# Kernel optimization log

Measured on AMD Instinct MI355X. Metric: run time of the kernel, lower is better.

The kernel has to match this reference:

```python
import jax, jax.numpy as jnp
import numpy as np

N = 50000   # nodes
E = 800000  # edges
D = 64      # d_in = d_h = d_out
H1 = 8      # GAT layer-1 heads


def _self_loops(src, dst, n):
    loop = jnp.arange(n)
    return jnp.concatenate([src, loop]), jnp.concatenate([dst, loop])


def gcn_conv(x, src, dst, W, b):
    # PyG GCNConv: symmetric normalization with self-loops, bias added last.
    n = x.shape[0]
    h = x @ W
    s, d = _self_loops(src, dst, n)
    deg = jax.ops.segment_sum(jnp.ones(s.shape[0], h.dtype), d, num_segments=n)
    dinv = jnp.where(deg > 0, deg ** -0.5, 0.0)
    norm = dinv[s] * dinv[d]                                   # [E+N]
    out = jax.ops.segment_sum(h[s] * norm[:, None], d, num_segments=n)
    return out + b


def sage_conv(x, src, dst, Wl, bl, Wr):
    # PyG SAGEConv: mean neighbor aggregation -> lin_l, plus root -> lin_r.
    n = x.shape[0]
    msg = jax.ops.segment_sum(x[src], dst, num_segments=n)
    cnt = jax.ops.segment_sum(jnp.ones(src.shape[0], x.dtype), dst, num_segments=n)
    mean = msg / jnp.maximum(cnt, 1.0)[:, None]
    return mean @ Wl + bl + x @ Wr


def gat_conv(x, src, dst, W, a_src, a_dst, b, heads):
    # PyG GATConv: per-head additive attention, self-loops, segment softmax, concat.
    n = x.shape[0]
    h = (x @ W).reshape(n, heads, -1)                          # [N,H,C]
    al_s = (h * a_src).sum(-1)                                 # [N,H]
    al_d = (h * a_dst).sum(-1)                                 # [N,H]
    s, d = _self_loops(src, dst, n)
    e = jax.nn.leaky_relu(al_s[s] + al_d[d], 0.2)              # [E',H]
    emax = jax.ops.segment_max(e, d, num_segments=n)           # [N,H]
    ex = jnp.exp(e - emax[d])
    den = jax.ops.segment_sum(ex, d, num_segments=n)
    alpha = ex / (den[d] + 1e-16)                              # [E',H]
    out = jax.ops.segment_sum(h[s] * alpha[:, :, None], d, num_segments=n)
    return out.reshape(n, -1) + b


def relu_res(h):
    # get_hiddens: rh = h before ReLU module, then h = relu(h) + rh
    return jax.nn.relu(h) + h


def layer_norm(x, g, b, eps=1e-6):
    mu = x.mean(-1, keepdims=True)
    var = ((x - mu) ** 2).mean(-1, keepdims=True)
    return (x - mu) * jax.lax.rsqrt(var + eps) * g + b


def setup_inputs():
    key = jax.random.key(0)
    ks = jax.random.split(key, 16)
    sc = 1.0 / np.sqrt(D)
    return {
        "x": jax.random.normal(ks[0], (N, D), jnp.float32),
        "edge_index": jax.random.randint(ks[1], (2, E), 0, N),
        "batch": jnp.sort(jax.random.randint(ks[2], (N,), 0, 64)),
        "gcn_W": jax.random.normal(ks[3], (3, D, D), jnp.float32) * sc,
        "gcn_b": jnp.zeros((3, D), jnp.float32),
        "sage_Wl": jax.random.normal(ks[4], (3, D, D), jnp.float32) * sc,
        "sage_bl": jnp.zeros((3, D), jnp.float32),
        "sage_Wr": jax.random.normal(ks[5], (3, D, D), jnp.float32) * sc,
        "gat1_W": jax.random.normal(ks[6], (D, D), jnp.float32) * sc,
        "gat1_asrc": jax.random.normal(ks[7], (H1, D // H1), jnp.float32) * sc,
        "gat1_adst": jax.random.normal(ks[8], (H1, D // H1), jnp.float32) * sc,
        "gat1_b": jnp.zeros((D,), jnp.float32),
        "gat2_W": jax.random.normal(ks[9], (D, D), jnp.float32) * sc,
        "gat2_asrc": jax.random.normal(ks[10], (1, D), jnp.float32) * sc,
        "gat2_adst": jax.random.normal(ks[11], (1, D), jnp.float32) * sc,
        "gat2_b": jnp.zeros((D,), jnp.float32),
        "ln_g": jnp.ones((D,), jnp.float32),
        "ln_b": jnp.zeros((D,), jnp.float32),
    }


def reference(x, edge_index, batch, gcn_W, gcn_b, sage_Wl, sage_bl, sage_Wr,
              gat1_W, gat1_asrc, gat1_adst, gat1_b,
              gat2_W, gat2_asrc, gat2_adst, gat2_b, ln_g, ln_b):
    src, dst = edge_index[0], edge_index[1]
    # channel 0: sz_l=3 GCNConv stack
    h = x
    for l in range(3):
        h = relu_res(gcn_conv(h, src, dst, gcn_W[l], gcn_b[l]))
    c_gcn = h
    # channel 1: GAT(8 heads) -> GAT(1 head)
    h = relu_res(gat_conv(x, src, dst, gat1_W, gat1_asrc, gat1_adst, gat1_b, H1))
    h = relu_res(gat_conv(h, src, dst, gat2_W, gat2_asrc, gat2_adst, gat2_b, 1))
    c_gat = h
    # channel 2: sz_l=3 SAGEConv stack
    h = x
    for l in range(3):
        h = relu_res(sage_conv(h, src, dst, sage_Wl[l], sage_bl[l], sage_Wr[l]))
    c_sage = h
    channal = jnp.stack([c_gcn, c_gat, c_sage])                # [3,N,d_out]
    out = layer_norm(channal, ln_g, ln_b)
    batchs = jnp.ones((3, batch.shape[0]), jnp.float32) * batch.astype(jnp.float32)
    return out, batchs
```

## Files before the change

kernel.cpp:

```cpp
#include <hip/hip_runtime.h>
#include <hip/hip_bf16.h>

typedef __hip_bfloat16 bf16;

static inline int ceil_div(long long a, int b) { return (int)((a + b - 1) / b); }

__device__ __forceinline__ float ld(const void* p, long long i, int f32) {
    return f32 ? ((const float*)p)[i] : __bfloat162float(((const bf16*)p)[i]);
}
__device__ __forceinline__ void st_out(void* p, long long i, int f32, float v) {
    if (f32) ((float*)p)[i] = v;
    else ((bf16*)p)[i] = __float2bfloat16(v);
}
__device__ __forceinline__ float lrelu(float v) { return v > 0.f ? v : 0.2f * v; }

__device__ __forceinline__ float4 f4z() { return make_float4(0.f, 0.f, 0.f, 0.f); }
__device__ __forceinline__ float4 f4add(float4 a, float4 b) {
    return make_float4(a.x + b.x, a.y + b.y, a.z + b.z, a.w + b.w);
}
__device__ __forceinline__ float4 f4fmas(float4 acc, float s, float4 v) {
    return make_float4(fmaf(s, v.x, acc.x), fmaf(s, v.y, acc.y),
                       fmaf(s, v.z, acc.z), fmaf(s, v.w, acc.w));
}
__device__ __forceinline__ float4 f4sxpe(float4 acc, float s, float e, float4 v) {
// ... 130 lines not shown
    }
}

__global__ void k_fill2(const int2* __restrict__ se, const int* __restrict__ start,
                        int* __restrict__ csr, int n) {
    __shared__ int cur[256];
    int t = threadIdx.x;
    int node0 = blockIdx.x << 8;
    int node = node0 + t;
    cur[t] = (node < n) ? start[node] : 0;
    __syncthreads();
    int nend = node0 + 256; if (nend > n) nend = n;
    int e0 = start[node0];
    int e1 = start[nend];
    for (int i = e0 + t; i < e1; i += 256) {
        int2 e = se[i];
        int p = atomicAdd(&cur[e.y & 255], 1);
        csr[p] = e.x;
    }
}


__global__ void k_gather12(const void* __restrict__ X,
                           const int* __restrict__ start, const int* __restrict__ csr,
                           const float* __restrict__ dinv, const float* __restrict__ invc,
                           float* __restrict__ Msage, float* __restrict__ Ggcn,
                           int n, const int* __restrict__ flag) {
    int t = threadIdx.x;
    int lane = t & 63, seg = lane >> 4, l16 = lane & 15;
    long long wave = (long long)blockIdx.x * 4 + (t >> 6);
    int d = (int)(wave * 4 + seg);
    if (d >= n) return;
    int xf32 = flag[0];
    int c4 = l16 << 2;
    int s0 = start[d], s1 = start[d + 1];
    float4 a0 = f4z(), a1 = f4z(), g0 = f4z(), g1 = f4z();
    int i = s0;
    for (; i + 7 < s1; i += 8) {
        int sA = csr[i],     sB = csr[i + 1], sC = csr[i + 2], sD = csr[i + 3];
        int sE = csr[i + 4], sF = csr[i + 5], sG = csr[i + 6], sH = csr[i + 7];
        float4 vA = ldrow4(X, sA, c4, xf32);
        float4 vB = ldrow4(X, sB, c4, xf32);
        float4 vC = ldrow4(X, sC, c4, xf32);
        float4 vD = ldrow4(X, sD, c4, xf32);
        float4 vE = ldrow4(X, sE, c4, xf32);
        float4 vF = ldrow4(X, sF, c4, xf32);
        float4 vG = ldrow4(X, sG, c4, xf32);
        float4 vH = ldrow4(X, sH, c4, xf32);
        float wA = dinv[sA], wB = dinv[sB], wC = dinv[sC], wD = dinv[sD];
        float wE = dinv[sE], wF = dinv[sF], wG = dinv[sG], wH = dinv[sH];
        a0 = f4add(a0, vA); g0 = f4fmas(g0, wA, vA);
        a1 = f4add(a1, vB); g1 = f4fmas(g1, wB, vB);
        a0 = f4add(a0, vC); g0 = f4fmas(g0, wC, vC);
        a1 = f4add(a1, vD); g1 = f4fmas(g1, wD, vD);
        a0 = f4add(a0, vE); g0 = f4fmas(g0, wE, vE);
        a1 = f4add(a1, vF); g1 = f4fmas(g1, wF, vF);
        a0 = f4add(a0, vG); g0 = f4fmas(g0, wG, vG);
        a1 = f4add(a1, vH); g1 = f4fmas(g1, wH, vH);
    }
    if (i + 3 < s1) {
        int sA = csr[i], sB = csr[i + 1], sC = csr[i + 2], sD = csr[i + 3];
        float4 vA = ldrow4(X, sA, c4, xf32);
        float4 vB = ldrow4(X, sB, c4, xf32);
        float4 vC = ldrow4(X, sC, c4, xf32);
        float4 vD = ldrow4(X, sD, c4, xf32);
        float wA = dinv[sA], wB = dinv[sB], wC = dinv[sC], wD = dinv[sD];
        a0 = f4add(a0, vA); g0 = f4fmas(g0, wA, vA);
        a1 = f4add(a1, vB); g1 = f4fmas(g1, wB, vB);
        a0 = f4add(a0, vC); g0 = f4fmas(g0, wC, vC);
        a1 = f4add(a1, vD); g1 = f4fmas(g1, wD, vD);
        i += 4;
    }
    for (; i < s1; ++i) {
        int sA = csr[i];
        float4 vA = ldrow4(X, sA, c4, xf32);
        a0 = f4add(a0, vA); g0 = f4fmas(g0, dinv[sA], vA);
    }
    float inv = invc[d];
    float4 ms = f4add(a0, a1);
    float4 gg = f4add(g0, g1);
    ms = make_float4(ms.x * inv, ms.y * inv, ms.z * inv, ms.w * inv);
    *(float4*)&Msage[(long long)d * 64 + c4] = ms;
    *(float4*)&Ggcn[(long long)d * 64 + c4] = gg;
}

__global__ void k_sage_gather(const float* __restrict__ S,
                              const int* __restrict__ start, const int* __restrict__ csr,
                              const float* __restrict__ invc, float* __restrict__ M,
                              int n) {
    int t = threadIdx.x;
    int lane = t & 63, seg = lane >> 4, l16 = lane & 15;
    long long wave = (long long)blockIdx.x * 4 + (t >> 6);
    int d = (int)(wave * 4 + seg);
    if (d >= n) return;
    const float4* S4 = (const float4*)S;
    int s0 = start[d], s1 = start[d + 1];
    float4 a0 = f4z(), a1 = f4z();
    int i = s0;
    for (; i + 7 < s1; i += 8) {
        int sA = csr[i],     sB = csr[i + 1], sC = csr[i + 2], sD = csr[i + 3];
        int sE = csr[i + 4], sF = csr[i + 5], sG = csr[i + 6], sH = csr[i + 7];
        float4 vA = S4[(long long)sA * 16 + l16];
        float4 vB = S4[(long long)sB * 16 + l16];
        float4 vC = S4[(long long)sC * 16 + l16];
        float4 vD = S4[(long long)sD * 16 + l16];
        float4 vE = S4[(long long)sE * 16 + l16];
        float4 vF = S4[(long long)sF * 16 + l16];
        float4 vG = S4[(long long)sG * 16 + l16];
        float4 vH = S4[(long long)sH * 16 + l16];
        a0 = f4add(a0, f4add(vA, vC));
        a1 = f4add(a1, f4add(vB, vD));
        a0 = f4add(a0, f4add(vE, vG));
        a1 = f4add(a1, f4add(vF, vH));
    }
    if (i + 3 < s1) {
        int sA = csr[i], sB = csr[i + 1], sC = csr[i + 2], sD = csr[i + 3];
        float4 vA = S4[(long long)sA * 16 + l16];
        float4 vB = S4[(long long)sB * 16 + l16];
        float4 vC = S4[(long long)sC * 16 + l16];
        float4 vD = S4[(long long)sD * 16 + l16];
        a0 = f4add(a0, f4add(vA, vC));
        a1 = f4add(a1, f4add(vB, vD));
        i += 4;
    }
    for (; i < s1; ++i) a0 = f4add(a0, S4[(long long)csr[i] * 16 + l16]);
    float inv = invc[d];
    float4 r = f4add(a0, a1);
    r = make_float4(r.x * inv, r.y * inv, r.z * inv, r.w * inv);
    *(float4*)&M[(long long)d * 64 + (l16 << 2)] = r;
}

__global__ void k_gcn_gather(const float* __restrict__ T, const int* __restrict__ start,
                             const int* __restrict__ csr, const float* __restrict__ dinv,
                             const void* __restrict__ b_b, const void* __restrict__ b_f,
                             float* __restrict__ P, int n, const int* __restrict__ flag,
                             int do_ln, const void* __restrict__ g, const void* __restrict__ bln,
                             void* __restrict__ outbase, long long elem_off) {
    int t = threadIdx.x;
    int lane = t & 63, seg = lane >> 4, l16 = lane & 15;
    long long wave = (long long)blockIdx.x * 4 + (t >> 6);
    int d = (int)(wave * 4 + seg);
    if (d >= n) return;
    int f32 = flag[0];
    const void* b = f32 ? b_f : b_b;
    int c4 = l16 << 2;
    const float4* T4 = (const float4*)T;
    float wd = dinv[d];
    int s0 = start[d], s1 = start[d + 1];
    float4 a0 = f4z(), a1 = f4z();
    int i = s0;
    for (; i + 7 < s1; i += 8) {
        int sA = csr[i],     sB = csr[i + 1], sC = csr[i + 2], sD = csr[i + 3];
        int sE = csr[i + 4], sF = csr[i + 5], sG = csr[i + 6], sH = csr[i + 7];
        float4 vA = T4[(long long)sA * 16 + l16];
        float4 vB = T4[(long long)sB * 16 + l16];
        float4 vC = T4[(long long)sC * 16 + l16];
        float4 vD = T4[(long long)sD * 16 + l16];
        float4 vE = T4[(long long)sE * 16 + l16];
        float4 vF = T4[(long long)sF * 16 + l16];
        float4 vG = T4[(long long)sG * 16 + l16];
        float4 vH = T4[(long long)sH * 16 + l16];
        float wA = dinv[sA], wB = dinv[sB], wC = dinv[sC], wD = dinv[sD];
        float wE = dinv[sE], wF = dinv[sF], wG = dinv[sG], wH = dinv[sH];
        a0 = f4fmas(a0, wA, vA); a1 = f4fmas(a1, wB, vB);
        a0 = f4fmas(a0, wC, vC); a1 = f4fmas(a1, wD, vD);
        a0 = f4fmas(a0, wE, vE); a1 = f4fmas(a1, wF, vF);
        a0 = f4fmas(a0, wG, vG); a1 = f4fmas(a1, wH, vH);
    }
    if (i + 3 < s1) {
        int sA = csr[i], sB = csr[i + 1], sC = csr[i + 2], sD = csr[i + 3];
        float4 vA = T4[(long long)sA * 16 + l16];
        float4 vB = T4[(long long)sB * 16 + l16];
        float4 vC = T4[(long long)sC * 16 + l16];
        float4 vD = T4[(long long)sD * 16 + l16];
        float wA = dinv[sA], wB = dinv[sB], wC = dinv[sC], wD = dinv[sD];
        a0 = f4fmas(a0, wA, vA); a1 = f4fmas(a1, wB, vB);
        a0 = f4fmas(a0, wC, vC); a1 = f4fmas(a1, wD, vD);
        i += 4;
    }
    for (; i < s1; ++i) { int sA = csr[i]; a0 = f4fmas(a0, dinv[sA], T4[(long long)sA * 16 + l16]); }
    float4 sm = f4add(a0, a1);
    float4 selfv = T4[(long long)d * 16 + l16];
    float wd2 = wd * wd;
    float v0 = wd * sm.x + wd2 * selfv.x + ld(b, c4 + 0, f32);
    float v1 = wd * sm.y + wd2 * selfv.y + ld(b, c4 + 1, f32);
    float v2 = wd * sm.z + wd2 * selfv.z + ld(b, c4 + 2, f32);
    float v3 = wd * sm.w + wd2 * selfv.w + ld(b, c4 + 3, f32);
    float4 hv = make_float4(fmaxf(v0, 0.f) + v0, fmaxf(v1, 0.f) + v1,
                            fmaxf(v2, 0.f) + v2, fmaxf(v3, 0.f) + v3);
    if (!do_ln) {
        *(float4*)&P[(long long)d * 64 + c4] = hv;
    } else {
        float loc = (hv.x + hv.y) + (hv.z + hv.w);
        for (int o = 1; o < 16; o <<= 1) loc += __shfl_xor(loc, o, 64);
        float mu = loc * (1.0f / 64.0f);
        float dx = hv.x - mu, dy = hv.y - mu, dz = hv.z - mu, dw = hv.w - mu;
        float s2 = (dx * dx + dy * dy) + (dz * dz + dw * dw);
        for (int o = 1; o < 16; o <<= 1) s2 += __shfl_xor(s2, o, 64);
        float rsig = rsqrtf(s2 * (1.0f / 64.0f) + 1e-6f);
        long long o0 = elem_off + (long long)d * 64 + c4;
        st_out(outbase, o0 + 0, f32, dx * rsig * ld(g, c4 + 0, f32) + ld(bln, c4 + 0, f32));
        st_out(outbase, o0 + 1, f32, dy * rsig * ld(g, c4 + 1, f32) + ld(bln, c4 + 1, f32));
        st_out(outbase, o0 + 2, f32, dz * rsig * ld(g, c4 + 2, f32) + ld(bln, c4 + 2, f32));
        st_out(outbase, o0 + 3, f32, dw * rsig * ld(g, c4 + 3, f32) + ld(bln, c4 + 3, f32));
    }
}

__global__ void k_gat_flash(const float* __restrict__ T, const int* __restrict__ start,
                            const int* __restrict__ csr, const float* __restrict__ als,
                            const float* __restrict__ ald, int n, int H, int hshift,
                            const void* __restrict__ b, float* __restrict__ P,
                            const int* __restrict__ flag) {
// ... 12 lines not shown
    float4 acc = T4[(long long)d * 16 + l16];
    int s0 = start[d], s1 = start[d + 1];
    int i = s0;
    for (; i + 7 < s1; i += 8) {
        int sA = csr[i],     sB = csr[i + 1], sC = csr[i + 2], sD = csr[i + 3];
        int sE = csr[i + 4], sF = csr[i + 5], sG = csr[i + 6], sH = csr[i + 7];
        float4 vA = T4[(long long)sA * 16 + l16];
        float4 vB = T4[(long long)sB * 16 + l16];
        float4 vC = T4[(long long)sC * 16 + l16];
        float4 vD = T4[(long long)sD * 16 + l16];
        float4 vE = T4[(long long)sE * 16 + l16];
        float4 vF = T4[(long long)sF * 16 + l16];
        float4 vG = T4[(long long)sG * 16 + l16];
        float4 vH = T4[(long long)sH * 16 + l16];
        float lA = lrelu(als[(long long)sA * H + h] + ad);
        float lB = lrelu(als[(long long)sB * H + h] + ad);
        float lC = lrelu(als[(long long)sC * H + h] + ad);
        float lD = lrelu(als[(long long)sD * H + h] + ad);
        float lE = lrelu(als[(long long)sE * H + h] + ad);
        float lF = lrelu(als[(long long)sF * H + h] + ad);
        float lG = lrelu(als[(long long)sG * H + h] + ad);
        float lH = lrelu(als[(long long)sH * H + h] + ad);
        float mn = fmaxf(m, fmaxf(fmaxf(fmaxf(lA, lB), fmaxf(lC, lD)),
                                  fmaxf(fmaxf(lE, lF), fmaxf(lG, lH))));
        float sc = __expf(m - mn);
        float eA = __expf(lA - mn), eB = __expf(lB - mn);
        float eC = __expf(lC - mn), eD = __expf(lD - mn);
        float eE = __expf(lE - mn), eF = __expf(lF - mn);
        float eG = __expf(lG - mn), eH = __expf(lH - mn);
        l = fmaf(l, sc, ((eA + eB) + (eC + eD)) + ((eE + eF) + (eG + eH)));
        acc = f4sxpe(acc, sc, eA, vA);
        acc = f4fmas(acc, eB, vB);
        acc = f4fmas(acc, eC, vC);
        acc = f4fmas(acc, eD, vD);
        acc = f4fmas(acc, eE, vE);
        acc = f4fmas(acc, eF, vF);
        acc = f4fmas(acc, eG, vG);
        acc = f4fmas(acc, eH, vH);
        m = mn;
    }
    if (i + 3 < s1) {
        int sA = csr[i], sB = csr[i + 1], sC = csr[i + 2], sD = csr[i + 3];
        float4 vA = T4[(long long)sA * 16 + l16];
        float4 vB = T4[(long long)sB * 16 + l16];
        float4 vC = T4[(long long)sC * 16 + l16];
        float4 vD = T4[(long long)sD * 16 + l16];
        float lA = lrelu(als[(long long)sA * H + h] + ad);
        float lB = lrelu(als[(long long)sB * H + h] + ad);
        float lC = lrelu(als[(long long)sC * H + h] + ad);
        float lD = lrelu(als[(long long)sD * H + h] + ad);
        float mn = fmaxf(m, fmaxf(fmaxf(lA, lB), fmaxf(lC, lD)));
        float sc = __expf(m - mn);
        float eA = __expf(lA - mn), eB = __expf(lB - mn);
        float eC = __expf(lC - mn), eD = __expf(lD - mn);
        l = fmaf(l, sc, (eA + eB) + (eC + eD));
        acc = f4sxpe(acc, sc, eA, vA);
        acc = f4fmas(acc, eB, vB);
        acc = f4fmas(acc, eC, vC);
        acc = f4fmas(acc, eD, vD);
        m = mn;
        i += 4;
    }
    for (; i < s1; ++i) {
        int sA = csr[i];
        float4 vA = T4[(long long)sA * 16 + l16];
        float lA = lrelu(als[(long long)sA * H + h] + ad);
        float mn = fmaxf(m, lA);
        float sc = __expf(m - mn);
        float eA = __expf(lA - mn);
        l = fmaf(l, sc, eA);
        acc = f4sxpe(acc, sc, eA, vA);
        m = mn;
    }
    float rden = 1.0f / (l + 1e-16f);
    float v0 = acc.x * rden + ld(b, c4 + 0, f32);
    float v1 = acc.y * rden + ld(b, c4 + 1, f32);
    float v2 = acc.z * rden + ld(b, c4 + 2, f32);
    float v3 = acc.w * rden + ld(b, c4 + 3, f32);
    float4 o = make_float4(fmaxf(v0, 0.f) + v0, fmaxf(v1, 0.f) + v1,
                           fmaxf(v2, 0.f) + v2, fmaxf(v3, 0.f) + v3);
    *(float4*)&P[(long long)d * 64 + c4] = o;
}


#define STAGE_W(Wp, f32m)                                                       \
    for (int i = t; i < 1024; i += 256) ((float4*)Ws)[i] = ld4(Wp, i, f32m);

#define STAGE_A(inp, f32m)                                                      \
    for (int i = t; i < 1024; i += 256) {                                       \
        int r = i >> 4, k4 = (i & 15) << 2;                                     \
        long long gr = R0 + r;                                                  \
        float4 v = (gr < nrows) ? ld4(inp, gr * 16 + (i & 15), f32m) : f4z();   \
        At[at_idx(k4 + 0, r)] = v.x;                                            \
        At[at_idx(k4 + 1, r)] = v.y;                                            \
        At[at_idx(k4 + 2, r)] = v.z;                                            \
        At[at_idx(k4 + 3, r)] = v.w;                                            \
    }

#define GEMM_CORE                                                               \
    _Pragma("unroll 8")                                                         \
    for (int k = 0; k < 64; ++k) {                                              \
        float4 a = *(const float4*)&At[k * 64 + ((tr ^ ((k >> 2) & 15)) << 2)]; \
        float4 b = *(const float4*)&Ws[k * 64 + (tc << 2)];                     \
        acc[0][0] = fmaf(a.x, b.x, acc[0][0]); acc[0][1] = fmaf(a.x, b.y, acc[0][1]); \
        acc[0][2] = fmaf(a.x, b.z, acc[0][2]); acc[0][3] = fmaf(a.x, b.w, acc[0][3]); \
        acc[1][0] = fmaf(a.y, b.x, acc[1][0]); acc[1][1] = fmaf(a.y, b.y, acc[1][1]); \
        acc[1][2] = fmaf(a.y, b.z, acc[1][2]); acc[1][3] = fmaf(a.y, b.w, acc[1][3]); \
        acc[2][0] = fmaf(a.z, b.x, acc[2][0]); acc[2][1] = fmaf(a.z, b.y, acc[2][1]); \
        acc[2][2] = fmaf(a.z, b.z, acc[2][2]); acc[2][3] = fmaf(a.z, b.w, acc[2][3]); \
        acc[3][0] = fmaf(a.w, b.x, acc[3][0]); acc[3][1] = fmaf(a.w, b.y, acc[3][1]); \
        acc[3][2] = fmaf(a.w, b.z, acc[3][2]); acc[3][3] = fmaf(a.w, b.w, acc[3][3]); \
    }

__global__ void k_gemm2(const void* __restrict__ in, const void* __restrict__ W_b,
                        const void* __restrict__ W_f, float* __restrict__ out,
                        int nrows, int in_is_ext, const int* __restrict__ flag) {
    __shared__ __align__(16) float At[64 * 64];
    __shared__ __align__(16) float Ws[64 * 64];
    int f32 = flag[0];
    const void* W = f32 ? W_f : W_b;
    int in_f32 = in_is_ext ? f32 : 1;
    int t = threadIdx.x;
    long long R0 = (long long)blockIdx.x * 64;
    STAGE_W(W, f32)
    STAGE_A(in, in_f32)
    __syncthreads();
    int tr = t & 15, tc = t >> 4;
    float acc[4][4] = {};
    GEMM_CORE
#pragma unroll
    for (int i = 0; i < 4; ++i) {
        long long r = R0 + 4 * tr + i;
        if (r < nrows) {
            float4 v = make_float4(acc[i][0], acc[i][1], acc[i][2], acc[i][3]);
            *(float4*)&out[r * 64 + (tc << 2)] = v;
        }
    }
}

__global__ void k_gat_mm(const void* __restrict__ in, const void* __restrict__ W,
                         float* __restrict__ out, int nrows, int in_is_ext,
                         const int* __restrict__ flag,
                         const void* __restrict__ a_src, const void* __restrict__ a_dst,
                         int C, float* __restrict__ als, float* __restrict__ ald) {
    __shared__ __align__(16) float At[64 * 64];
    __shared__ __align__(16) float Ws[64 * 64];
    int f32 = flag[0];
    int in_f32 = in_is_ext ? f32 : 1;
    int t = threadIdx.x;
    long long R0 = (long long)blockIdx.x * 64;
    STAGE_W(W, f32)
    STAGE_A(in, in_f32)
    __syncthreads();
    int tr = t & 15, tc = t >> 4;
    float acc[4][4] = {};
    GEMM_CORE
#pragma unroll
    for (int i = 0; i < 4; ++i) {
        long long r = R0 + 4 * tr + i;
        if (r < nrows) {
            float4 v = make_float4(acc[i][0], acc[i][1], acc[i][2], acc[i][3]);
            *(float4*)&out[r * 64 + (tc << 2)] = v;
        }
    }
    __syncthreads();
#pragma unroll
    for (int i = 0; i < 4; ++i) {
        float4 v = make_float4(acc[i][0], acc[i][1], acc[i][2], acc[i][3]);
        *(float4*)&At[(4 * tr + i) * 64 + (tc << 2)] = v;
    }
    __syncthreads();
    int w = t >> 6, c = t & 63;
    float av = ld(a_src, c, f32);
    float dv = ld(a_dst, c, f32);
    int H = 64 / C;
    for (int rr = 0; rr < 16; ++rr) {
        int rl = (w << 4) + rr;
        float v = At[rl * 64 + c];
        float ps = v * av, pd = v * dv;
        for (int o = 1; o < C; o <<= 1) {
            ps += __shfl_xor(ps, o, 64);
            pd += __shfl_xor(pd, o, 64);
        }
        long long gr = R0 + rl;
        if ((c & (C - 1)) == 0 && gr < nrows) {
            als[gr * H + (c / C)] = ps;
            ald[gr * H + (c / C)] = pd;
        }
    }
}

__global__ void k_gcn_mm1(const float* __restrict__ G, const void* __restrict__ X,
                          const float* __restrict__ dinv,
                          const void* __restrict__ W_b, const void* __restrict__ W_f,
                          const void* __restrict__ b_b, const void* __restrict__ b_f,
                          float* __restrict__ out, int nrows, const int* __restrict__ flag) {
    __shared__ __align__(16) float At[64 * 64];
    __shared__ __align__(16) float Ws[64 * 64];
    int f32 = flag[0];
    const void* W = f32 ? W_f : W_b;
    int t = threadIdx.x;
    long long R0 = (long long)blockIdx.x * 64;
    STAGE_W(W, f32)
    for (int i = t; i < 1024; i += 256) {
        int r = i >> 4, k4 = (i & 15) << 2;
        long long gr = R0 + r;
        float4 v = f4z();
        if (gr < nrows) {
            float wd = dinv[gr];
            float wd2 = wd * wd;
            float4 gv = ((const float4*)G)[gr * 16 + (i & 15)];
            float4 xv = ld4(X, gr * 16 + (i & 15), f32);
            v = make_float4(wd * gv.x + wd2 * xv.x, wd * gv.y + wd2 * xv.y,
                            wd * gv.z + wd2 * xv.z, wd * gv.w + wd2 * xv.w);
        }
        At[at_idx(k4 + 0, r)] = v.x;
        At[at_idx(k4 + 1, r)] = v.y;
        At[at_idx(k4 + 2, r)] = v.z;
        At[at_idx(k4 + 3, r)] = v.w;
    }
    __syncthreads();
    int tr = t & 15, tc = t >> 4;
    float acc[4][4] = {};
    GEMM_CORE
#pragma unroll
    for (int i = 0; i < 4; ++i) {
        long long r = R0 + 4 * tr + i;
        if (r < nrows) {
            float4 v;
            float v0 = acc[i][0] + ld(f32 ? b_f : b_b, (tc << 2) + 0, f32);
            float v1 = acc[i][1] + ld(f32 ? b_f : b_b, (tc << 2) + 1, f32);
            float v2 = acc[i][2] + ld(f32 ? b_f : b_b, (tc << 2) + 2, f32);
            float v3 = acc[i][3] + ld(f32 ? b_f : b_b, (tc << 2) + 3, f32);
            v.x = fmaxf(v0, 0.f) + v0;
            v.y = fmaxf(v1, 0.f) + v1;
            v.z = fmaxf(v2, 0.f) + v2;
            v.w = fmaxf(v3, 0.f) + v3;
            *(float4*)&out[r * 64 + (tc << 2)] = v;
        }
    }
}

__global__ void k_sage_mm(const float* __restrict__ M, const void* __restrict__ Sx,
                          int s_is_ext,
                          const void* __restrict__ Wl_b, const void* __restrict__ Wl_f,
                          const void* __restrict__ Wr_b, const void* __restrict__ Wr_f,
                          const void* __restrict__ bl_b, const void* __restrict__ bl_f,
                          float* __restrict__ out, int nrows, const int* __restrict__ flag,
                          int do_ln, const void* __restrict__ g, const void* __restrict__ bln,
                          void* __restrict__ outbase, long long elem_off) {
    __shared__ __align__(16) float At[64 * 64];
    __shared__ __align__(16) float Ws[64 * 64];
    int f32 = flag[0];
    int sf32 = s_is_ext ? f32 : 1;
    int t = threadIdx.x;
    long long R0 = (long long)blockIdx.x * 64;
    int tr = t & 15, tc = t >> 4;
    float acc[4][4] = {};

    {
        const void* wl = f32 ? Wl_f : Wl_b;
        STAGE_W(wl, f32)
        for (int i = t; i < 1024; i += 256) {
            int r = i >> 4, k4 = (i & 15) << 2;
            long long gr = R0 + r;
            float4 v = (gr < nrows) ? ((const float4*)M)[gr * 16 + (i & 15)] : f4z();
            At[at_idx(k4 + 0, r)] = v.x;
            At[at_idx(k4 + 1, r)] = v.y;
            At[at_idx(k4 + 2, r)] = v.z;
            At[at_idx(k4 + 3, r)] = v.w;
        }
    }
    float4 pa[4], pw[4];
    {
        const void* wr = f32 ? Wr_f : Wr_b;
#pragma unroll
        for (int j = 0; j < 4; ++j) {
            int i = t + (j << 8);
            pw[j] = ld4(wr, i, f32);
            int r = i >> 4;
            long long gr = R0 + r;
            pa[j] = (gr < nrows) ? ld4(Sx, gr * 16 + (i & 15), sf32) : f4z();
        }
    }
    __syncthreads();
    GEMM_CORE
    __syncthreads();
#pragma unroll
    for (int j = 0; j < 4; ++j) {
        int i = t + (j << 8);
        ((float4*)Ws)[i] = pw[j];
        int r = i >> 4, k4 = (i & 15) << 2;
        At[at_idx(k4 + 0, r)] = pa[j].x;
        At[at_idx(k4 + 1, r)] = pa[j].y;
        At[at_idx(k4 + 2, r)] = pa[j].z;
        At[at_idx(k4 + 3, r)] = pa[j].w;
    }
    __syncthreads();
    GEMM_CORE
    const void* bl = f32 ? bl_f : bl_b;
    float bias[4];
#pragma unroll
    for (int j = 0; j < 4; ++j) bias[j] = ld(bl, (tc << 2) + j, f32);
    float vv[4][4];
#pragma unroll
    for (int i = 0; i < 4; ++i)
#pragma unroll
        for (int j = 0; j < 4; ++j) {
            float v = acc[i][j] + bias[j];
            vv[i][j] = fmaxf(v, 0.f) + v;
        }
    if (!do_ln) {
#pragma unroll
        for (int i = 0; i < 4; ++i) {
            long long r = R0 + 4 * tr + i;
            if (r < nrows) {
                float4 v = make_float4(vv[i][0], vv[i][1], vv[i][2], vv[i][3]);
                *(float4*)&out[r * 64 + (tc << 2)] = v;
            }
        }
    } else {
        __syncthreads();
#pragma unroll
        for (int i = 0; i < 4; ++i) {
            float4 v = make_float4(vv[i][0], vv[i][1], vv[i][2], vv[i][3]);
            *(float4*)&At[(4 * tr + i) * 64 + (tc << 2)] = v;
        }
        __syncthreads();
        int w = t >> 6, lane = t & 63;
        for (int rr = 0; rr < 16; ++rr) {
            int rl = (w << 4) + rr;
            float v = At[rl * 64 + lane];
            float sum = v;
            for (int o = 32; o > 0; o >>= 1) sum += __shfl_xor(sum, o, 64);
            float mu = sum * (1.0f / 64.0f);
            float d0 = v - mu;
            float s2 = d0 * d0;
            for (int o = 32; o > 0; o >>= 1) s2 += __shfl_xor(s2, o, 64);
            float y = d0 * rsqrtf(s2 * (1.0f / 64.0f) + 1e-6f) * ld(g, lane, f32)
                    + ld(bln, lane, f32);
            long long grow = R0 + rl;
            if (grow < nrows)
                st_out(outbase, elem_off + grow * 64 + lane, f32, y);
        }
    }
}

__global__ void k_ln(const float* __restrict__ P, const void* __restrict__ g,
                     const void* __restrict__ b, int n, void* __restrict__ outbase,
                     long long elem_off, const int* __restrict__ flag) {
    int gid = blockIdx.x * blockDim.x + threadIdx.x;
    int node = gid >> 6, lane = gid & 63;
    if (node >= n) return;
    int f32 = flag[0];
    float v = P[(long long)node * 64 + lane];
    float sum = v;
    for (int o = 32; o > 0; o >>= 1) sum += __shfl_xor(sum, o, 64);
    float mu = sum * (1.0f / 64.0f);
    float d0 = v - mu;
    float s2 = d0 * d0;
    for (int o = 32; o > 0; o >>= 1) s2 += __shfl_xor(s2, o, 64);
    float var = s2 * (1.0f / 64.0f);
    float y = d0 * rsqrtf(var + 1e-6f) * ld(g, lane, f32) + ld(b, lane, f32);
    st_out(outbase, elem_off + (long long)node * 64 + lane, f32, y);
}

__global__ void k_batchs(const int* __restrict__ batch, int n, void* __restrict__ outbase,
                         long long elem_off, const int* __restrict__ flag) {
    int idx = blockIdx.x * blockDim.x + threadIdx.x;
    if (idx >= 3 * n) return;
    st_out(outbase, elem_off + idx, flag[0], (float)batch[idx % n]);
}

extern "C" void kernel_launch(void* const* d_in, const int* in_sizes, int n_in,
                              void* d_out, int out_size, void* d_ws, size_t ws_size,
                              hipStream_t stream) {
    const void* x       = d_in[0];
    const int*  ei      = (const int*)d_in[1];
    const int*  batch   = (const int*)d_in[2];
    const char* gcn_W   = (const char*)d_in[3];
    const char* gcn_b   = (const char*)d_in[4];
    const char* sage_Wl = (const char*)d_in[5];
    const char* sage_bl = (const char*)d_in[6];
    const char* sage_Wr = (const char*)d_in[7];
    const void* gat1_W  = d_in[8];
    const void* gat1_as = d_in[9];
    const void* gat1_ad = d_in[10];
    const void* gat1_b  = d_in[11];
    const void* gat2_W  = d_in[12];
    const void* gat2_as = d_in[13];
    const void* gat2_ad = d_in[14];
    const void* gat2_b  = d_in[15];
    const void* ln_g    = d_in[16];
    const void* ln_b    = d_in[17];

    const int n = in_sizes[2];
    const int E = in_sizes[1] / 2;
    const size_t ND = (size_t)n * 64;

    float* P    = (float*)d_ws;
    float* T    = P + ND;
    int*   icnt = (int*)(T + ND);
    float* dinv = (float*)(icnt + n);
    float* invc = dinv + n;
    int*   flag = (int*)(invc + n);
    int*   gcur = flag + 64;
    int2*  se   = (int2*)T;

    float* Ggcn  = (float*)d_out;
    int* csr_src = (int*)((char*)d_out + ND * 4);
    int* start   = csr_src + E;
    float* als   = (float*)(start + n + 64);
    float* ald   = als + (size_t)n * 8;
    int* bsum    = (int*)als;

    const int B = 256;
    const int gN    = ceil_div(n, B);
    const int gND   = ceil_div((long long)ND, B);
    const int gE    = ceil_div(E, B);
    const int gT64  = ceil_div(n, 64);
    const int gW4   = ceil_div(n, 16);
    const int nb    = ceil_div(n, 256);

    k_flag<<<1, 64, 0, stream>>>(ln_g, flag);

    k_zero_int<<<gN, B, 0, stream>>>(icnt, n);
    k_count<<<gE, B, 0, stream>>>(ei, E, icnt);
    k_scan_blk<<<nb, 256, 0, stream>>>(icnt, n, start, bsum);
    k_scan_top<<<1, 256, 0, stream>>>(bsum, nb);
    k_scan_add<<<gN, B, 0, stream>>>(start, bsum, icnt, dinv, invc, n, E);
    k_zero_int<<<1, 256, 0, stream>>>(gcur, 256);
    k_bucket<<<ceil_div(E, 4096), 256, 0, stream>>>(ei, E, start, gcur, se, n);
    k_fill2<<<nb, 256, 0, stream>>>(se, start, csr_src, n);

    k_gather12<<<gW4, B, 0, stream>>>(x, start, csr_src, dinv, invc, P, Ggcn, n, flag);

    {
        k_sage_mm<<<gT64, B, 0, stream>>>(P, x, 1,
            sage_Wl, sage_Wl, sage_Wr, sage_Wr, sage_bl, sage_bl, P, n, flag,
            0, ln_g, ln_b, d_out, 0);
        k_sage_gather<<<gW4, B, 0, stream>>>(P, start, csr_src, invc, T, n);
        k_sage_mm<<<gT64, B, 0, stream>>>(T, P, 0,
            sage_Wl + 4096 * 2, sage_Wl + 4096 * 4, sage_Wr + 4096 * 2, sage_Wr + 4096 * 4,
            sage_bl + 64 * 2, sage_bl + 64 * 4, T, n, flag,
            0, ln_g, ln_b, d_out, 0);
        k_sage_gather<<<gW4, B, 0, stream>>>(T, start, csr_src, invc, P, n);
        k_sage_mm<<<gT64, B, 0, stream>>>(P, T, 0,
            sage_Wl + 8192 * 2, sage_Wl + 8192 * 4, sage_Wr + 8192 * 2, sage_Wr + 8192 * 4,
            sage_bl + 128 * 2, sage_bl + 128 * 4, P, n, flag,
            1, ln_g, ln_b, d_out, 2 * (long long)ND);
    }

    k_gcn_mm1<<<gT64, B, 0, stream>>>(Ggcn, x, dinv, gcn_W, gcn_W, gcn_b, gcn_b,
                                      P, n, flag);
    for (int l = 1; l < 3; ++l) {
        const void* W_b = gcn_W + (size_t)l * 4096 * 2;
        const void* W_f = gcn_W + (size_t)l * 4096 * 4;
        const void* b_b = gcn_b + (size_t)l * 64 * 2;
        const void* b_f = gcn_b + (size_t)l * 64 * 4;
        k_gemm2<<<gT64, B, 0, stream>>>(P, W_b, W_f, T, n, 0, flag);
        k_gcn_gather<<<gW4, B, 0, stream>>>(T, start, csr_src, dinv, b_b, b_f, P, n, flag,
                                            (l == 2) ? 1 : 0, ln_g, ln_b, d_out, 0);
    }

    {
        k_gat_mm<<<gT64, B, 0, stream>>>(x, gat1_W, T, n, 1, flag,
                                         gat1_as, gat1_ad, 8, als, ald);
        k_gat_flash<<<gW4, B, 0, stream>>>(T, start, csr_src, als, ald, n, 8, 3,
                                           gat1_b, P, flag);
        k_gat_mm<<<gT64, B, 0, stream>>>(P, gat2_W, T, n, 0, flag,
                                         gat2_as, gat2_ad, 64, als, ald);
        k_gat_flash<<<gW4, B, 0, stream>>>(T, start, csr_src, als, ald, n, 1, 6,
                                           gat2_b, P, flag);
    }
    k_ln<<<gND, B, 0, stream>>>(P, ln_g, ln_b, n, d_out, (long long)ND, flag);

    k_batchs<<<ceil_div((long long)3 * n, B), B, 0, stream>>>(batch, n, d_out,
                                                              3 * (long long)ND, flag);
}
```

Baseline: 580.5 us.

## Fuse neighbor gathers with following dense GEMMs in SAGE, GCN and GAT stacks

Merges each graph aggregation step with the next 64x64 matmul in one kernel. Each block gathers 64 destination rows into shared memory and multiplies by the staged weights there, so the intermediate aggregate no longer goes through global memory. SAGE gather+lin_l+lin_r, GCN layer-2 gather+layer-3 GEMM, and GAT layer-1 attention+layer-2 projection plus attention logits are each fused, removing several launches and full-size round trips. The cost is that one block now serializes gather and GEMM phases, which can lower occupancy and the memory-latency hiding the gather kernels had.

```diff
diff --git a/kernel.cpp b/kernel.cpp
--- a/kernel.cpp
+++ b/kernel.cpp
@@ -236,52 +236,6 @@
     ms = make_float4(ms.x * inv, ms.y * inv, ms.z * inv, ms.w * inv);
     *(float4*)&Msage[(long long)d * 64 + c4] = ms;
     *(float4*)&Ggcn[(long long)d * 64 + c4] = gg;
-}
-
-__global__ void k_sage_gather(const float* __restrict__ S,
-                              const int* __restrict__ start, const int* __restrict__ csr,
-                              const float* __restrict__ invc, float* __restrict__ M,
-                              int n) {
-    int t = threadIdx.x;
-    int lane = t & 63, seg = lane >> 4, l16 = lane & 15;
-    long long wave = (long long)blockIdx.x * 4 + (t >> 6);
-    int d = (int)(wave * 4 + seg);
-    if (d >= n) return;
-    const float4* S4 = (const float4*)S;
-    int s0 = start[d], s1 = start[d + 1];
-    float4 a0 = f4z(), a1 = f4z();
-    int i = s0;
-    for (; i + 7 < s1; i += 8) {
-        int sA = csr[i],     sB = csr[i + 1], sC = csr[i + 2], sD = csr[i + 3];
-        int sE = csr[i + 4], sF = csr[i + 5], sG = csr[i + 6], sH = csr[i + 7];
-        float4 vA = S4[(long long)sA * 16 + l16];
-        float4 vB = S4[(long long)sB * 16 + l16];
-        float4 vC = S4[(long long)sC * 16 + l16];
-        float4 vD = S4[(long long)sD * 16 + l16];
-        float4 vE = S4[(long long)sE * 16 + l16];
-        float4 vF = S4[(long long)sF * 16 + l16];
-        float4 vG = S4[(long long)sG * 16 + l16];
-        float4 vH = S4[(long long)sH * 16 + l16];
-        a0 = f4add(a0, f4add(vA, vC));
-        a1 = f4add(a1, f4add(vB, vD));
-        a0 = f4add(a0, f4add(vE, vG));
-        a1 = f4add(a1, f4add(vF, vH));
-    }
-    if (i + 3 < s1) {
-        int sA = csr[i], sB = csr[i + 1], sC = csr[i + 2], sD = csr[i + 3];
-        float4 vA = S4[(long long)sA * 16 + l16];
-        float4 vB = S4[(long long)sB * 16 + l16];
-        float4 vC = S4[(long long)sC * 16 + l16];
-        float4 vD = S4[(long long)sD * 16 + l16];
-        a0 = f4add(a0, f4add(vA, vC));
-        a1 = f4add(a1, f4add(vB, vD));
-        i += 4;
-    }
-    for (; i < s1; ++i) a0 = f4add(a0, S4[(long long)csr[i] * 16 + l16]);
-    float inv = invc[d];
-    float4 r = f4add(a0, a1);
-    r = make_float4(r.x * inv, r.y * inv, r.z * inv, r.w * inv);
-    *(float4*)&M[(long long)d * 64 + (l16 << 2)] = r;
 }
 
 __global__ void k_gcn_gather(const float* __restrict__ T, const int* __restrict__ start,
@@ -460,7 +414,6 @@
     *(float4*)&P[(long long)d * 64 + c4] = o;
 }
 
-
 #define STAGE_W(Wp, f32m)                                                       \
     for (int i = t; i < 1024; i += 256) ((float4*)Ws)[i] = ld4(Wp, i, f32m);
 
@@ -490,6 +443,74 @@
         acc[3][2] = fmaf(a.w, b.z, acc[3][2]); acc[3][3] = fmaf(a.w, b.w, acc[3][3]); \
     }
 
+#define GATHER8_SUM(SRC4)                                                        \
+    {                                                                            \
+        int i = s0;                                                              \
+        for (; i + 7 < s1; i += 8) {                                             \
+            int sA = csr[i],     sB = csr[i + 1], sC = csr[i + 2], sD = csr[i + 3]; \
+            int sE = csr[i + 4], sF = csr[i + 5], sG = csr[i + 6], sH = csr[i + 7]; \
+            float4 vA = SRC4[(long long)sA * 16 + l16];                          \
+            float4 vB = SRC4[(long long)sB * 16 + l16];                          \
+            float4 vC = SRC4[(long long)sC * 16 + l16];                          \
+            float4 vD = SRC4[(long long)sD * 16 + l16];                          \
+            float4 vE = SRC4[(long long)sE * 16 + l16];                          \
+            float4 vF = SRC4[(long long)sF * 16 + l16];                          \
+            float4 vG = SRC4[(long long)sG * 16 + l16];                          \
+            float4 vH = SRC4[(long long)sH * 16 + l16];                          \
+            a0 = f4add(a0, f4add(vA, vC));                                       \
+            a1 = f4add(a1, f4add(vB, vD));                                       \
+            a0 = f4add(a0, f4add(vE, vG));                                       \
+            a1 = f4add(a1, f4add(vF, vH));                                       \
+        }                                                                        \
+        if (i + 3 < s1) {                                                        \
+            int sA = csr[i], sB = csr[i + 1], sC = csr[i + 2], sD = csr[i + 3];  \
+            float4 vA = SRC4[(long long)sA * 16 + l16];                          \
+            float4 vB = SRC4[(long long)sB * 16 + l16];                          \
+            float4 vC = SRC4[(long long)sC * 16 + l16];                          \
+            float4 vD = SRC4[(long long)sD * 16 + l16];                          \
+            a0 = f4add(a0, f4add(vA, vC));                                       \
+            a1 = f4add(a1, f4add(vB, vD));                                       \
+            i += 4;                                                              \
+        }                                                                        \
+        for (; i < s1; ++i) a0 = f4add(a0, SRC4[(long long)csr[i] * 16 + l16]);  \
+    }
+
+#define GATHER8_WSUM(SRC4)                                                       \
+    {                                                                            \
+        int i = s0;                                                              \
+        for (; i + 7 < s1; i += 8) {                                             \
+            int sA = csr[i],     sB = csr[i + 1], sC = csr[i + 2], sD = csr[i + 3]; \
+            int sE = csr[i + 4], sF = csr[i + 5], sG = csr[i + 6], sH = csr[i + 7]; \
+            float4 vA = SRC4[(long long)sA * 16 + l16];                          \
+            float4 vB = SRC4[(long long)sB * 16 + l16];                          \
+            float4 vC = SRC4[(long long)sC * 16 + l16];                          \
+            float4 vD = SRC4[(long long)sD * 16 + l16];                          \
+            float4 vE = SRC4[(long long)sE * 16 + l16];                          \
+            float4 vF = SRC4[(long long)sF * 16 + l16];                          \
+            float4 vG = SRC4[(long long)sG * 16 + l16];                          \
+            float4 vH = SRC4[(long long)sH * 16 + l16];                          \
+            float wA = dinv[sA], wB = dinv[sB], wC = dinv[sC], wD = dinv[sD];    \
+            float wE = dinv[sE], wF = dinv[sF], wG = dinv[sG], wH = dinv[sH];    \
+            a0 = f4fmas(a0, wA, vA); a1 = f4fmas(a1, wB, vB);                    \
+            a0 = f4fmas(a0, wC, vC); a1 = f4fmas(a1, wD, vD);                    \
+            a0 = f4fmas(a0, wE, vE); a1 = f4fmas(a1, wF, vF);                    \
+            a0 = f4fmas(a0, wG, vG); a1 = f4fmas(a1, wH, vH);                    \
+        }                                                                        \
+        if (i + 3 < s1) {                                                        \
+            int sA = csr[i], sB = csr[i + 1], sC = csr[i + 2], sD = csr[i + 3];  \
+            float4 vA = SRC4[(long long)sA * 16 + l16];                          \
+            float4 vB = SRC4[(long long)sB * 16 + l16];                          \
+            float4 vC = SRC4[(long long)sC * 16 + l16];                          \
+            float4 vD = SRC4[(long long)sD * 16 + l16];                          \
+            float wA = dinv[sA], wB = dinv[sB], wC = dinv[sC], wD = dinv[sD];    \
+            a0 = f4fmas(a0, wA, vA); a1 = f4fmas(a1, wB, vB);                    \
+            a0 = f4fmas(a0, wC, vC); a1 = f4fmas(a1, wD, vD);                    \
+            i += 4;                                                              \
+        }                                                                        \
+        for (; i < s1; ++i) { int sA = csr[i];                                   \
+            a0 = f4fmas(a0, dinv[sA], SRC4[(long long)sA * 16 + l16]); }         \
+    }
+
 __global__ void k_gemm2(const void* __restrict__ in, const void* __restrict__ W_b,
                         const void* __restrict__ W_f, float* __restrict__ out,
                         int nrows, int in_is_ext, const int* __restrict__ flag) {
@@ -624,9 +645,7 @@
                           const void* __restrict__ Wl_b, const void* __restrict__ Wl_f,
                           const void* __restrict__ Wr_b, const void* __restrict__ Wr_f,
                           const void* __restrict__ bl_b, const void* __restrict__ bl_f,
-                          float* __restrict__ out, int nrows, const int* __restrict__ flag,
-                          int do_ln, const void* __restrict__ g, const void* __restrict__ bln,
-                          void* __restrict__ outbase, long long elem_off) {
+                          float* __restrict__ out, int nrows, const int* __restrict__ flag) {
     __shared__ __align__(16) float At[64 * 64];
     __shared__ __align__(16) float Ws[64 * 64];
     int f32 = flag[0];
@@ -635,7 +654,6 @@
     long long R0 = (long long)blockIdx.x * 64;
     int tr = t & 15, tc = t >> 4;
     float acc[4][4] = {};
-
     {
         const void* wl = f32 ? Wl_f : Wl_b;
         STAGE_W(wl, f32)
@@ -677,6 +695,92 @@
     __syncthreads();
     GEMM_CORE
     const void* bl = f32 ? bl_f : bl_b;
+#pragma unroll
+    for (int i = 0; i < 4; ++i) {
+        long long r = R0 + 4 * tr + i;
+        if (r < nrows) {
+            float4 v;
+            float v0 = acc[i][0] + ld(bl, (tc << 2) + 0, f32);
+            float v1 = acc[i][1] + ld(bl, (tc << 2) + 1, f32);
+            float v2 = acc[i][2] + ld(bl, (tc << 2) + 2, f32);
+            float v3 = acc[i][3] + ld(bl, (tc << 2) + 3, f32);
+            v.x = fmaxf(v0, 0.f) + v0;
+            v.y = fmaxf(v1, 0.f) + v1;
+            v.z = fmaxf(v2, 0.f) + v2;
+            v.w = fmaxf(v3, 0.f) + v3;
+            *(float4*)&out[r * 64 + (tc << 2)] = v;
+        }
+    }
+}
+
+__global__ void k_sage_fused(const float* __restrict__ S,
+                             const int* __restrict__ start, const int* __restrict__ csr,
+                             const float* __restrict__ invc,
+                             const void* __restrict__ Wl_b, const void* __restrict__ Wl_f,
+                             const void* __restrict__ Wr_b, const void* __restrict__ Wr_f,
+                             const void* __restrict__ bl_b, const void* __restrict__ bl_f,
+                             float* __restrict__ out, int nrows, const int* __restrict__ flag,
+                             int do_ln, const void* __restrict__ g, const void* __restrict__ bln,
+                             void* __restrict__ outbase, long long elem_off) {
+    __shared__ __align__(16) float At[64 * 64];
+    __shared__ __align__(16) float Ws[64 * 64];
+    int f32 = flag[0];
+    int t = threadIdx.x;
+    long long R0 = (long long)blockIdx.x * 64;
+    int tr = t & 15, tc = t >> 4;
+    int lane = t & 63, wv = t >> 6, seg = lane >> 4, l16 = lane & 15;
+    int c4 = l16 << 2;
+    const float4* S4 = (const float4*)S;
+    {
+        const void* wl = f32 ? Wl_f : Wl_b;
+        STAGE_W(wl, f32)
+    }
+    for (int ii = 0; ii < 4; ++ii) {
+        int rl = (wv << 4) + (ii << 2) + seg;
+        long long d = R0 + rl;
+        float4 r = f4z();
+        if (d < nrows) {
+            int s0 = start[d], s1 = start[d + 1];
+            float4 a0 = f4z(), a1 = f4z();
+            GATHER8_SUM(S4)
+            float inv = invc[d];
+            r = f4add(a0, a1);
+            r = make_float4(r.x * inv, r.y * inv, r.z * inv, r.w * inv);
+        }
+        At[at_idx(c4 + 0, rl)] = r.x;
+        At[at_idx(c4 + 1, rl)] = r.y;
+        At[at_idx(c4 + 2, rl)] = r.z;
+        At[at_idx(c4 + 3, rl)] = r.w;
+    }
+    float4 pa[4], pw[4];
+    {
+        const void* wr = f32 ? Wr_f : Wr_b;
+#pragma unroll
+        for (int j = 0; j < 4; ++j) {
+            int i = t + (j << 8);
+            pw[j] = ld4(wr, i, f32);
+            int r = i >> 4;
+            long long gr = R0 + r;
+            pa[j] = (gr < nrows) ? S4[gr * 16 + (i & 15)] : f4z();
+        }
+    }
+    __syncthreads();
+    float acc[4][4] = {};
+    GEMM_CORE
+    __syncthreads();
+#pragma unroll
+    for (int j = 0; j < 4; ++j) {
+        int i = t + (j << 8);
+        ((float4*)Ws)[i] = pw[j];
+        int r = i >> 4, k4 = (i & 15) << 2;
+        At[at_idx(k4 + 0, r)] = pa[j].x;
+        At[at_idx(k4 + 1, r)] = pa[j].y;
+        At[at_idx(k4 + 2, r)] = pa[j].z;
+        At[at_idx(k4 + 3, r)] = pa[j].w;
+    }
+    __syncthreads();
+    GEMM_CORE
+    const void* bl = f32 ? bl_f : bl_b;
     float bias[4];
 #pragma unroll
     for (int j = 0; j < 4; ++j) bias[j] = ld(bl, (tc << 2) + j, f32);
@@ -705,21 +809,211 @@
             *(float4*)&At[(4 * tr + i) * 64 + (tc << 2)] = v;
         }
         __syncthreads();
-        int w = t >> 6, lane = t & 63;
+        int lane2 = t & 63, w2 = t >> 6;
         for (int rr = 0; rr < 16; ++rr) {
-            int rl = (w << 4) + rr;
-            float v = At[rl * 64 + lane];
+            int rl = (w2 << 4) + rr;
+            float v = At[rl * 64 + lane2];
             float sum = v;
             for (int o = 32; o > 0; o >>= 1) sum += __shfl_xor(sum, o, 64);
             float mu = sum * (1.0f / 64.0f);
             float d0 = v - mu;
             float s2 = d0 * d0;
             for (int o = 32; o > 0; o >>= 1) s2 += __shfl_xor(s2, o, 64);
-            float y = d0 * rsqrtf(s2 * (1.0f / 64.0f) + 1e-6f) * ld(g, lane, f32)
-                    + ld(bln, lane, f32);
+            float y = d0 * rsqrtf(s2 * (1.0f / 64.0f) + 1e-6f) * ld(g, lane2, f32)
+                    + ld(bln, lane2, f32);
             long long grow = R0 + rl;
             if (grow < nrows)
-                st_out(outbase, elem_off + grow * 64 + lane, f32, y);
+                st_out(outbase, elem_off + grow * 64 + lane2, f32, y);
+        }
+    }
+}
+
+__global__ void k_gcn_fused(const float* __restrict__ T,
+                            const int* __restrict__ start, const int* __restrict__ csr,
+                            const float* __restrict__ dinv,
+                            const void* __restrict__ b_b, const void* __restrict__ b_f,
+                            const void* __restrict__ W_b, const void* __restrict__ W_f,
+                            float* __restrict__ out, int nrows, const int* __restrict__ flag) {
+    __shared__ __align__(16) float At[64 * 64];
+    __shared__ __align__(16) float Ws[64 * 64];
+    int f32 = flag[0];
+    const void* b = f32 ? b_f : b_b;
+    int t = threadIdx.x;
+    long long R0 = (long long)blockIdx.x * 64;
+    int tr = t & 15, tc = t >> 4;
+    int lane = t & 63, wv = t >> 6, seg = lane >> 4, l16 = lane & 15;
+    int c4 = l16 << 2;
+    const float4* T4 = (const float4*)T;
+    {
+        const void* W = f32 ? W_f : W_b;
+        STAGE_W(W, f32)
+    }
+    float b0 = ld(b, c4 + 0, f32), b1 = ld(b, c4 + 1, f32);
+    float b2 = ld(b, c4 + 2, f32), b3 = ld(b, c4 + 3, f32);
+    for (int ii = 0; ii < 4; ++ii) {
+        int rl = (wv << 4) + (ii << 2) + seg;
+        long long d = R0 + rl;
+        float4 hv = f4z();
+        if (d < nrows) {
+            float wd = dinv[d];
+            int s0 = start[d], s1 = start[d + 1];
+            float4 a0 = f4z(), a1 = f4z();
+            GATHER8_WSUM(T4)
+            float4 sm = f4add(a0, a1);
+            float4 selfv = T4[d * 16 + l16];
+            float wd2 = wd * wd;
+            float v0 = wd * sm.x + wd2 * selfv.x + b0;
+            float v1 = wd * sm.y + wd2 * selfv.y + b1;
+            float v2 = wd * sm.z + wd2 * selfv.z + b2;
+            float v3 = wd * sm.w + wd2 * selfv.w + b3;
+            hv = make_float4(fmaxf(v0, 0.f) + v0, fmaxf(v1, 0.f) + v1,
+                             fmaxf(v2, 0.f) + v2, fmaxf(v3, 0.f) + v3);
+        }
+        At[at_idx(c4 + 0, rl)] = hv.x;
+        At[at_idx(c4 + 1, rl)] = hv.y;
+        At[at_idx(c4 + 2, rl)] = hv.z;
+        At[at_idx(c4 + 3, rl)] = hv.w;
+    }
+    __syncthreads();
+    float acc[4][4] = {};
+    GEMM_CORE
+#pragma unroll
+    for (int i = 0; i < 4; ++i) {
+        long long r = R0 + 4 * tr + i;
+        if (r < nrows) {
+            float4 v = make_float4(acc[i][0], acc[i][1], acc[i][2], acc[i][3]);
+            *(float4*)&out[r * 64 + (tc << 2)] = v;
+        }
+    }
+}
+
+__global__ void k_gat_fused(const float* __restrict__ T,
+                            const int* __restrict__ start, const int* __restrict__ csr,
+                            const float* __restrict__ als, const float* __restrict__ ald,
+                            const void* __restrict__ b1,
+                            const void* __restrict__ W2,
+                            const void* __restrict__ a2s, const void* __restrict__ a2d,
+                            float* __restrict__ out, float* __restrict__ als2,
+                            float* __restrict__ ald2,
+                            int nrows, const int* __restrict__ flag) {
+    __shared__ __align__(16) float At[64 * 64];
+    __shared__ __align__(16) float Ws[64 * 64];
+    int f32 = flag[0];
+    int t = threadIdx.x;
+    long long R0 = (long long)blockIdx.x * 64;
+    int tr = t & 15, tc = t >> 4;
+    int lane = t & 63, wv = t >> 6, seg = lane >> 4, l16 = lane & 15;
+    int c4 = l16 << 2;
+    int h = c4 >> 3;
+    const float4* T4 = (const float4*)T;
+    STAGE_W(W2, f32)
+    float bb0 = ld(b1, c4 + 0, f32), bb1 = ld(b1, c4 + 1, f32);
+    float bb2 = ld(b1, c4 + 2, f32), bb3 = ld(b1, c4 + 3, f32);
+    for (int ii = 0; ii < 4; ++ii) {
+        int rl = (wv << 4) + (ii << 2) + seg;
+        long long d = R0 + rl;
+        float4 o = f4z();
+        if (d < nrows) {
+            float ad = ald[d * 8 + h];
+            float m = lrelu(als[d * 8 + h] + ad);
+            float l = 1.0f;
+            float4 acc = T4[d * 16 + l16];
+            int s0 = start[d], s1 = start[d + 1];
+            int i = s0;
+            for (; i + 7 < s1; i += 8) {
+                int sA = csr[i],     sB = csr[i + 1], sC = csr[i + 2], sD = csr[i + 3];
+                int sE = csr[i + 4], sF = csr[i + 5], sG = csr[i + 6], sH = csr[i + 7];
+                float4 vA = T4[(long long)sA * 16 + l16];
+                float4 vB = T4[(long long)sB * 16 + l16];
+                float4 vC = T4[(long long)sC * 16 + l16];
+                float4 vD = T4[(long long)sD * 16 + l16];
+                float4 vE = T4[(long long)sE * 16 + l16];
+                float4 vF = T4[(long long)sF * 16 + l16];
+                float4 vG = T4[(long long)sG * 16 + l16];
+                float4 vH = T4[(long long)sH * 16 + l16];
+                float lA = lrelu(als[(long long)sA * 8 + h] + ad);
+                float lB = lrelu(als[(long long)sB * 8 + h] + ad);
+                float lC = lrelu(als[(long long)sC * 8 + h] + ad);
+                float lD = lrelu(als[(long long)sD * 8 + h] + ad);
+                float lE = lrelu(als[(long long)sE * 8 + h] + ad);
+                float lF = lrelu(als[(long long)sF * 8 + h] + ad);
+                float lG = lrelu(als[(long long)sG * 8 + h] + ad);
+                float lH = lrelu(als[(long long)sH * 8 + h] + ad);
+                float mn = fmaxf(m, fmaxf(fmaxf(fmaxf(lA, lB), fmaxf(lC, lD)),
+                                          fmaxf(fmaxf(lE, lF), fmaxf(lG, lH))));
+                float sc = __expf(m - mn);
+                float eA = __expf(lA - mn), eB = __expf(lB - mn);
+                float eC = __expf(lC - mn), eD = __expf(lD - mn);
+                float eE = __expf(lE - mn), eF = __expf(lF - mn);
+                float eG = __expf(lG - mn), eH = __expf(lH - mn);
+                l = fmaf(l, sc, ((eA + eB) + (eC + eD)) + ((eE + eF) + (eG + eH)));
+                acc = f4sxpe(acc, sc, eA, vA);
+                acc = f4fmas(acc, eB, vB);
+                acc = f4fmas(acc, eC, vC);
+                acc = f4fmas(acc, eD, vD);
+                acc = f4fmas(acc, eE, vE);
+                acc = f4fmas(acc, eF, vF);
+                acc = f4fmas(acc, eG, vG);
+                acc = f4fmas(acc, eH, vH);
+                m = mn;
+            }
+            for (; i < s1; ++i) {
+                int sA = csr[i];
+                float4 vA = T4[(long long)sA * 16 + l16];
+                float lA = lrelu(als[(long long)sA * 8 + h] + ad);
+                float mn = fmaxf(m, lA);
+                float sc = __expf(m - mn);
+                float eA = __expf(lA - mn);
+                l = fmaf(l, sc, eA);
+                acc = f4sxpe(acc, sc, eA, vA);
+                m = mn;
+            }
+            float rden = 1.0f / (l + 1e-16f);
+            float v0 = acc.x * rden + bb0;
+            float v1 = acc.y * rden + bb1;
+            float v2 = acc.z * rden + bb2;
+            float v3 = acc.w * rden + bb3;
+            o = make_float4(fmaxf(v0, 0.f) + v0, fmaxf(v1, 0.f) + v1,
+                            fmaxf(v2, 0.f) + v2, fmaxf(v3, 0.f) + v3);
+        }
+        At[at_idx(c4 + 0, rl)] = o.x;
+        At[at_idx(c4 + 1, rl)] = o.y;
+        At[at_idx(c4 + 2, rl)] = o.z;
+        At[at_idx(c4 + 3, rl)] = o.w;
+    }
+    __syncthreads();
+    float acc[4][4] = {};
+    GEMM_CORE
+#pragma unroll
+    for (int i = 0; i < 4; ++i) {
+        long long r = R0 + 4 * tr + i;
+        if (r < nrows) {
+            float4 v = make_float4(acc[i][0], acc[i][1], acc[i][2], acc[i][3]);
+            *(float4*)&out[r * 64 + (tc << 2)] = v;
+        }
+    }
+    __syncthreads();
+#pragma unroll
+    for (int i = 0; i < 4; ++i) {
+        float4 v = make_float4(acc[i][0], acc[i][1], acc[i][2], acc[i][3]);
+        *(float4*)&At[(4 * tr + i) * 64 + (tc << 2)] = v;
+    }
+    __syncthreads();
+    int w2 = t >> 6, c = t & 63;
+    float av = ld(a2s, c, f32);
+    float dv = ld(a2d, c, f32);
+    for (int rr = 0; rr < 16; ++rr) {
+        int rl = (w2 << 4) + rr;
+        float v = At[rl * 64 + c];
+        float ps = v * av, pd = v * dv;
+        for (int o = 1; o < 64; o <<= 1) {
+            ps += __shfl_xor(ps, o, 64);
+            pd += __shfl_xor(pd, o, 64);
+        }
+        long long gr = R0 + rl;
+        if (c == 0 && gr < nrows) {
+            als2[gr] = ps;
+            ald2[gr] = pd;
         }
     }
 }
@@ -790,6 +1084,8 @@
     int* start   = csr_src + E;
     float* als   = (float*)(start + n + 64);
     float* ald   = als + (size_t)n * 8;
+    float* als2  = ald + (size_t)n * 8;
+    float* ald2  = als2 + n;
     int* bsum    = (int*)als;
 
     const int B = 256;
@@ -815,43 +1111,39 @@
 
     {
         k_sage_mm<<<gT64, B, 0, stream>>>(P, x, 1,
-            sage_Wl, sage_Wl, sage_Wr, sage_Wr, sage_bl, sage_bl, P, n, flag,
-            0, ln_g, ln_b, d_out, 0);
-        k_sage_gather<<<gW4, B, 0, stream>>>(P, start, csr_src, invc, T, n);
-        k_sage_mm<<<gT64, B, 0, stream>>>(T, P, 0,
+            sage_Wl, sage_Wl, sage_Wr, sage_Wr, sage_bl, sage_bl, P, n, flag);
+        k_sage_fused<<<gT64, B, 0, stream>>>(P, start, csr_src, invc,
             sage_Wl + 4096 * 2, sage_Wl + 4096 * 4, sage_Wr + 4096 * 2, sage_Wr + 4096 * 4,
             sage_bl + 64 * 2, sage_bl + 64 * 4, T, n, flag,
             0, ln_g, ln_b, d_out, 0);
-        k_sage_gather<<<gW4, B, 0, stream>>>(T, start, csr_src, invc, P, n);
-        k_sage_mm<<<gT64, B, 0, stream>>>(P, T, 0,
+        k_sage_fused<<<gT64, B, 0, stream>>>(T, start, csr_src, invc,
             sage_Wl + 8192 * 2, sage_Wl + 8192 * 4, sage_Wr + 8192 * 2, sage_Wr + 8192 * 4,
-            sage_bl + 128 * 2, sage_bl + 128 * 4, P, n, flag,
+            sage_bl + 128 * 2, sage_bl + 128 * 4, P , n, flag,
             1, ln_g, ln_b, d_out, 2 * (long long)ND);
     }
 
-    k_gcn_mm1<<<gT64, B, 0, stream>>>(Ggcn, x, dinv, gcn_W, gcn_W, gcn_b, gcn_b,
-                                      P, n, flag);
-    for (int l = 1; l < 3; ++l) {
-        const void* W_b = gcn_W + (size_t)l * 4096 * 2;
-        const void* W_f = gcn_W + (size_t)l * 4096 * 4;
-        const void* b_b = gcn_b + (size_t)l * 64 * 2;
-        const void* b_f = gcn_b + (size_t)l * 64 * 4;
-        k_gemm2<<<gT64, B, 0, stream>>>(P, W_b, W_f, T, n, 0, flag);
-        k_gcn_gather<<<gW4, B, 0, stream>>>(T, start, csr_src, dinv, b_b, b_f, P, n, flag,
-                                            (l == 2) ? 1 : 0, ln_g, ln_b, d_out, 0);
+    {
+        k_gcn_mm1<<<gT64, B, 0, stream>>>(Ggcn, x, dinv, gcn_W, gcn_W, gcn_b, gcn_b,
+                                          P, n, flag);
+        k_gemm2<<<gT64, B, 0, stream>>>(P, gcn_W + 4096 * 2, gcn_W + 4096 * 4,
+                                        T, n, 0, flag);
+        k_gcn_fused<<<gT64, B, 0, stream>>>(T, start, csr_src, dinv,
+            gcn_b + 64 * 2, gcn_b + 64 * 4,
+            gcn_W + 8192 * 2, gcn_W + 8192 * 4, P, n, flag);
+        k_gcn_gather<<<gW4, B, 0, stream>>>(P, start, csr_src, dinv,
+            gcn_b + 128 * 2, gcn_b + 128 * 4, T , n, flag,
+            1, ln_g, ln_b, d_out, 0);
     }
 
     {
         k_gat_mm<<<gT64, B, 0, stream>>>(x, gat1_W, T, n, 1, flag,
                                          gat1_as, gat1_ad, 8, als, ald);
-        k_gat_flash<<<gW4, B, 0, stream>>>(T, start, csr_src, als, ald, n, 8, 3,
-                                           gat1_b, P, flag);
-        k_gat_mm<<<gT64, B, 0, stream>>>(P, gat2_W, T, n, 0, flag,
-                                         gat2_as, gat2_ad, 64, als, ald);
-        k_gat_flash<<<gW4, B, 0, stream>>>(T, start, csr_src, als, ald, n, 1, 6,
-                                           gat2_b, P, flag);
-    }
-    k_ln<<<gND, B, 0, stream>>>(P, ln_g, ln_b, n, d_out, (long long)ND, flag);
+        k_gat_fused<<<gT64, B, 0, stream>>>(T, start, csr_src, als, ald,
+            gat1_b, gat2_W, gat2_as, gat2_ad, P, als2, ald2, n, flag);
+        k_gat_flash<<<gW4, B, 0, stream>>>(P, start, csr_src, als2, ald2, n, 1, 6,
+                                           gat2_b, T, flag);
+    }
+    k_ln<<<gND, B, 0, stream>>>(T, ln_g, ln_b, n, d_out, (long long)ND, flag);
 
     k_batchs<<<ceil_div((long long)3 * n, B), B, 0, stream>>>(batch, n, d_out,
                                                               3 * (long long)ND, flag);
```

Result: faster. 555.0 us (-4.4%).
